# Optimization experiments

Measured on AMD Instinct MI355X. Metric: run time of the kernel, lower is better.

## Reference

```python
import jax, jax.numpy as jnp
import numpy as np

EPS = 1e-8
TOP_K = 3  # hardcoded in the original forward (torch.topk(sims, 3))


def setup_inputs() -> dict:
    key = jax.random.key(0)
    ks = jax.random.split(key, 6)
    n1, d1 = 4096, 1024
    n2, d2 = 4096, 4096
    V = jax.random.normal(ks[0], (n1, d1), dtype=jnp.float32)
    X = jax.random.normal(ks[1], (n2, d2), dtype=jnp.float32)
    # nn.Linear(visual_dim, text_dim): weight [d2, d1], bias [d2]
    Wv = jax.random.normal(ks[2], (d2, d1), dtype=jnp.float32) * (1.0 / np.sqrt(d1))
    bv = jax.random.normal(ks[3], (d2,), dtype=jnp.float32) * 0.01
    # nn.Linear(top_k, 1): weight [1, 3], bias [1]
    Wf = jax.random.normal(ks[4], (1, TOP_K), dtype=jnp.float32) * (1.0 / np.sqrt(TOP_K))
    bf = jax.random.normal(ks[5], (1,), dtype=jnp.float32) * 0.01
    return {"V": V, "X": X, "Wv": Wv, "bv": bv, "Wf": Wf, "bf": bf}


def reference(V, X, Wv, bv, Wf, bf):
    # project visual tokens into text space: [n1, d2]
    V_proj = V @ Wv.T + bv
    # cosine similarity: normalize queries (full-vector norm) and keys (row norm)
    Qn = X / (jnp.linalg.norm(X, axis=1, keepdims=True) + EPS)          # [n2, d2]
    Kn = V_proj / (jnp.linalg.norm(V_proj, axis=1, keepdims=True) + EPS)  # [n1, d2]
    sims = Qn @ Kn.T                                                     # [n2, n1]
    # per-text-token top-k visual tokens
    _, topk_idx = jax.lax.top_k(sims, TOP_K)                             # [n2, k]
    gathered = V_proj[topk_idx]                                          # [n2, k, d2]
    # fuse over k: Linear(k -> 1) applied along the top-k axis, squeeze -> [n2, d2]
    V_aligned = jnp.einsum('nkd,k->nd', gathered, Wf[0]) + bf[0]
    return jnp.concatenate([V_aligned, X], axis=0)                       # [2*n2, d2]
```

## Files before the change

kernel.cpp:

```cpp
#include <hip/hip_runtime.h>
#include <hip/hip_bf16.h>

constexpr int N1 = 4096;
constexpr int D1 = 1024;
constexpr int N2 = 4096;
constexpr int D2 = 4096;

#define FNEG  (-3.402823466e+38f)
#define IDX_INF 0x7FFFFFFF
#define NCHUNK 32
#define CPR (NCHUNK * 6)
#define FCAP 512
#define CERT_TH 1.5e-3f

using s16x8 = __attribute__((ext_vector_type(8))) short;
using f32x4 = __attribute__((ext_vector_type(4))) float;

static __device__ __forceinline__ unsigned short f2bf(float x) {
    unsigned int u = __float_as_uint(x);
    unsigned int r = (u + 0x7FFFu + ((u >> 16) & 1u)) >> 16;
    return (unsigned short)r;
}
static __device__ __forceinline__ float bf2f(unsigned short v) {
    return __uint_as_float((unsigned)v << 16);
}
static __device__ __forceinline__ void splitbf(float x, unsigned short& h,
                                               unsigned short& l) {
    unsigned short hh = f2bf(x);
    float r = x - __uint_as_float((unsigned)hh << 16);
    h = hh; l = f2bf(r);
}
static __device__ __forceinline__ int swz(int row, int g) {
    return row * 32 + ((g ^ (row & 3)) << 3);
}

static __device__ __forceinline__ void stageF32(const float* src, int ld,
    int rowbase, int k0, unsigned short* H, unsigned short* L, int tid)
{
    const int r = tid >> 1, half = tid & 1;
    const float* p = src + (size_t)(rowbase + r) * ld + k0 + half * 16;
#pragma unroll
    for (int gg = 0; gg < 2; ++gg) {
        const int g = half * 2 + gg;
        float4 v0 = *(const float4*)(p + gg * 8);
        float4 v1 = *(const float4*)(p + gg * 8 + 4);
        float xs[8] = {v0.x, v0.y, v0.z, v0.w, v1.x, v1.y, v1.z, v1.w};
        s16x8 hv, lv;
#pragma unroll
        for (int e = 0; e < 8; ++e) {
            unsigned short h, l; splitbf(xs[e], h, l);
            hv[e] = (short)h; lv[e] = (short)l;
        }
        const int a = swz(r, g);
        *(s16x8*)&H[a] = hv;
        *(s16x8*)&L[a] = lv;
    }
}

static __device__ __forceinline__ void gl_lds16(const void* g, void* l)
{
    __builtin_amdgcn_global_load_lds(
        (const __attribute__((address_space(1))) void*)g,
        (__attribute__((address_space(3))) void*)l, 16, 0, 0);
}

static __device__ __forceinline__ void stageSplitGL(const unsigned short* Hs,
    const unsigned short* Ls, int ld, int rowbase, int k0,
    unsigned short* H, unsigned short* L, int lane, int w)
{
#pragma unroll
    for (int t = 0; t < 2; ++t) {
        const int chunk = w * 128 + t * 64 + lane;
        const int row = chunk >> 2;
        const int gp  = chunk & 3;
        const int g   = gp ^ (row & 3);
        const unsigned short* sh =
            Hs + (size_t)(rowbase + row) * ld + k0 + g * 8;
        const unsigned short* sl =
            Ls + (size_t)(rowbase + row) * ld + k0 + g * 8;
        unsigned short* dh = H + (size_t)(w * 128 + t * 64) * 8;
        unsigned short* dl = L + (size_t)(w * 128 + t * 64) * 8;
        gl_lds16(sh, dh);
        gl_lds16(sl, dl);
    }
}

static __device__ __forceinline__ void stageWvTpre(const unsigned short* Wh,
    const unsigned short* Wl, int k0, int tn,
    unsigned short* H, unsigned short* L, int tid)
{
    const int kk = tid >> 3, cg = tid & 7;
    const int g = kk >> 3, idx = kk & 7;
    const unsigned short* ph = Wh + (size_t)(k0 + kk) * D1 + tn + cg * 16;
    const unsigned short* pl = Wl + (size_t)(k0 + kk) * D1 + tn + cg * 16;
#pragma unroll
    for (int q = 0; q < 4; ++q) {
        ushort4 vh = *(const ushort4*)(ph + q * 4);
        ushort4 vl = *(const ushort4*)(pl + q * 4);
        unsigned short hs[4] = {vh.x, vh.y, vh.z, vh.w};
        unsigned short ls[4] = {vl.x, vl.y, vl.z, vl.w};
#pragma unroll
        for (int e = 0; e < 4; ++e) {
            const int cc = cg * 16 + q * 4 + e;
            const int a = cc * 32 + ((g ^ (cc & 3)) << 3) + idx;
            H[a] = hs[e]; L[a] = ls[e];
        }
    }
}

static __device__ __forceinline__ s16x8 fragRead(const unsigned short* B,
                                                 int rowbase, int lane)
{
    const int row = rowbase + (lane & 15);
    const int g = lane >> 4;
    return *(const s16x8*)&B[row * 32 + ((g ^ (row & 3)) << 3)];
}

#define MFMA3(ACC, AH, AL, BH, BL)                                          \
    ACC = __builtin_amdgcn_mfma_f32_16x16x32_bf16(AH, BH, ACC, 0, 0, 0);    \
    ACC = __builtin_amdgcn_mfma_f32_16x16x32_bf16(AH, BL, ACC, 0, 0, 0);    \
    ACC = __builtin_amdgcn_mfma_f32_16x16x32_bf16(AL, BH, ACC, 0, 0, 0);

static __device__ __forceinline__ void top6f(float v, int i, float* vv, int* ii)
{
#pragma unroll
    for (int s = 0; s < 6; ++s) {
        if (v > vv[s]) {
#pragma unroll
            for (int t = 5; t > s; --t) { vv[t] = vv[t-1]; ii[t] = ii[t-1]; }
            vv[s] = v; ii[s] = i;
            break;
        }
    }
}

__global__ __launch_bounds__(256)
void kDetect(const float* c1, const float* c2, int* flags, int* flagCnt)
{
    __shared__ float red[256];
    float d = 0.f;
    for (int i = threadIdx.x; i < 4096; i += 256) {
        float a = c1[i], b = c2[i];
        d += a * a - b * b;
    }
    red[threadIdx.x] = d;
    __syncthreads();
    for (int st = 128; st > 0; st >>= 1) {
        if (threadIdx.x < st) red[threadIdx.x] += red[threadIdx.x + st];
        __syncthreads();
    }
    if (threadIdx.x == 0) {
        flags[0] = (red[0] < 0.f) ? 1 : 0;
        flagCnt[0] = 0;
    }
}

__global__ __launch_bounds__(256)
void kSplit(const float* src, unsigned short* h, unsigned short* l, int n4)
{
    int i = blockIdx.x * 256 + threadIdx.x;
    if (i >= n4) return;
    float4 v = *(const float4*)(src + (size_t)i * 4);
    float xs[4] = {v.x, v.y, v.z, v.w};
    ushort4 hv, lv;
    unsigned short hh, ll;
    splitbf(xs[0], hh, ll); hv.x = hh; lv.x = ll;
    splitbf(xs[1], hh, ll); hv.y = hh; lv.y = ll;
    splitbf(xs[2], hh, ll); hv.z = hh; lv.z = ll;
    splitbf(xs[3], hh, ll); hv.w = hh; lv.w = ll;
    *(ushort4*)(h + (size_t)i * 4) = hv;
    *(ushort4*)(l + (size_t)i * 4) = lv;
}

__global__ __launch_bounds__(256)
void kSvec(const float* X, const float* bv, float* sXF)
{
    __shared__ double red[256];
    const int row = blockIdx.x;
    double s = 0.0;
    for (int n = threadIdx.x; n < D2; n += 256)
        s += (double)X[(size_t)row * D2 + n] * (double)bv[n];
    red[threadIdx.x] = s;
    __syncthreads();
    for (int st = 128; st > 0; st >>= 1) {
        if (threadIdx.x < st) red[threadIdx.x] += red[threadIdx.x + st];
        __syncthreads();
    }
    if (threadIdx.x == 0) sXF[row] = (float)red[0];
}

__global__ __launch_bounds__(256)
void kNormMfma(const unsigned short* c1h, const unsigned short* c1l,
               const unsigned short* c2h, const unsigned short* c2l,
               const float* bv, const int* flags, float* partial,
               unsigned short* Vph)
{
    const unsigned short* Vh  = flags[0] ? c2h : c1h;
    const unsigned short* Vl  = flags[0] ? c2l : c1l;
    const unsigned short* Wvh = flags[0] ? c1h : c2h;
    const unsigned short* Wvl = flags[0] ? c1l : c2l;
    __shared__ unsigned short AH[4096], AL[4096], BH[4096], BL[4096];
    __shared__ float partH[128][2];
    const int tid = threadIdx.x;
    const int lane = tid & 63, w = tid >> 6;
    const int wr = w >> 1, wc = w & 1;
    const int tm = blockIdx.y * 128;
    const int tn = blockIdx.x * 128;

    f32x4 acc[4][4];
#pragma unroll
    for (int i = 0; i < 4; ++i)
#pragma unroll
        for (int j = 0; j < 4; ++j) acc[i][j] = (f32x4){0.f, 0.f, 0.f, 0.f};

    for (int k0 = 0; k0 < D1; k0 += 32) {
        stageSplitGL(Vh,  Vl,  D1, tm, k0, AH, AL, lane, w);
        stageSplitGL(Wvh, Wvl, D1, tn, k0, BH, BL, lane, w);
        __syncthreads();
        s16x8 ah[4], al[4], bh[4], bl[4];
#pragma unroll
        for (int f = 0; f < 4; ++f) {
            ah[f] = fragRead(AH, wr * 64 + f * 16, lane);
            al[f] = fragRead(AL, wr * 64 + f * 16, lane);
            bh[f] = fragRead(BH, wc * 64 + f * 16, lane);
            bl[f] = fragRead(BL, wc * 64 + f * 16, lane);
        }
#pragma unroll
        for (int fm = 0; fm < 4; ++fm)
#pragma unroll
            for (int fn = 0; fn < 4; ++fn) {
                MFMA3(acc[fm][fn], ah[fm], al[fm], bh[fn], bl[fn]);
            }
        __syncthreads();
    }

    float bvv[4];
#pragma unroll
    for (int fn = 0; fn < 4; ++fn)
        bvv[fn] = bv[tn + wc * 64 + fn * 16 + (lane & 15)];
#pragma unroll
    for (int fm = 0; fm < 4; ++fm)
#pragma unroll
        for (int r = 0; r < 4; ++r) {
            const int lrow = wr * 64 + fm * 16 + (lane >> 4) * 4 + r;
            float rs = 0.f;
#pragma unroll
            for (int fn = 0; fn < 4; ++fn) {
                float v = acc[fm][fn][r] + bvv[fn];
                Vph[(size_t)(tm + lrow) * D2 +
                    (tn + wc * 64 + fn * 16 + (lane & 15))] = f2bf(v);
                rs += v * v;
            }
            rs += __shfl_xor(rs, 1, 64);
            rs += __shfl_xor(rs, 2, 64);
            rs += __shfl_xor(rs, 4, 64);
            rs += __shfl_xor(rs, 8, 64);
            if ((lane & 15) == 0) partH[lrow][wc] = rs;
        }
    __syncthreads();
    if (tid < 128)
        partial[(size_t)(tm + tid) * 32 + blockIdx.x] =
            partH[tid][0] + partH[tid][1];
}

__global__ __launch_bounds__(256)
void kInv(const float* partial, float* invnF)
{
    int j = blockIdx.x * 256 + threadIdx.x;
    float s = 0.f;
    for (int cb = 0; cb < 32; ++cb) s += partial[(size_t)j * 32 + cb];
    invnF[j] = 1.f / (sqrtf(s) + 1e-8f);
}

__global__ __launch_bounds__(256)
void mfmaZ(const float* X,
           const unsigned short* c1h, const unsigned short* c1l,
           const unsigned short* c2h, const unsigned short* c2l,
           const int* flags, unsigned short* Zh, unsigned short* Zl)
{
    const unsigned short* Wvh = flags[0] ? c1h : c2h;
    const unsigned short* Wvl = flags[0] ? c1l : c2l;
    __shared__ unsigned short AH[4096], AL[4096], BH[4096], BL[4096];
    const int tid = threadIdx.x;
    const int lane = tid & 63, w = tid >> 6;
    const int wr = w >> 1, wc = w & 1;
    const int tm = blockIdx.y * 128;
    const int tn = blockIdx.x * 128;

    f32x4 acc[4][4];
#pragma unroll
    for (int i = 0; i < 4; ++i)
#pragma unroll
        for (int j = 0; j < 4; ++j) acc[i][j] = (f32x4){0.f, 0.f, 0.f, 0.f};

    for (int k0 = 0; k0 < D2; k0 += 32) {
        stageF32(X, D2, tm, k0, AH, AL, tid);
        stageWvTpre(Wvh, Wvl, k0, tn, BH, BL, tid);
        __syncthreads();
        s16x8 ah[4], al[4], bh[4], bl[4];
#pragma unroll
        for (int f = 0; f < 4; ++f) {
            ah[f] = fragRead(AH, wr * 64 + f * 16, lane);
            al[f] = fragRead(AL, wr * 64 + f * 16, lane);
            bh[f] = fragRead(BH, wc * 64 + f * 16, lane);
            bl[f] = fragRead(BL, wc * 64 + f * 16, lane);
        }
#pragma unroll
        for (int fm = 0; fm < 4; ++fm)
#pragma unroll
            for (int fn = 0; fn < 4; ++fn) {
                MFMA3(acc[fm][fn], ah[fm], al[fm], bh[fn], bl[fn]);
            }
        __syncthreads();
    }
#pragma unroll
    for (int fm = 0; fm < 4; ++fm)
#pragma unroll
        for (int fn = 0; fn < 4; ++fn)
#pragma unroll
            for (int r = 0; r < 4; ++r) {
                int row = tm + wr * 64 + fm * 16 + (lane >> 4) * 4 + r;
                int col = tn + wc * 64 + fn * 16 + (lane & 15);
                unsigned short h, l;
                splitbf(acc[fm][fn][r], h, l);
                size_t o = (size_t)row * D1 + col;
                Zh[o] = h; Zl[o] = l;
            }
}

__global__ __launch_bounds__(256)
void mfmaS(const unsigned short* Zh, const unsigned short* Zl,
           const unsigned short* c1h, const unsigned short* c1l,
           const unsigned short* c2h, const unsigned short* c2l,
           const float* invnF, const float* sXF, const int* flags,
           float* candV, int* candI)
{
    const unsigned short* Vh = flags[0] ? c2h : c1h;
    const unsigned short* Vl = flags[0] ? c2l : c1l;
    __shared__ __align__(16) char pool[41472];
    unsigned short* AH = (unsigned short*)pool;
    unsigned short* AL = (unsigned short*)(pool + 8192);
    unsigned short* BH = (unsigned short*)(pool + 16384);
    unsigned short* BL = (unsigned short*)(pool + 24576);
    float* Ct   = (float*)pool;
    float* pv   = (float*)(pool + 33792);
    int*   pi   = (int*)  (pool + 36864);
    float* invs = (float*)(pool + 39936);

    const int tid = threadIdx.x;
    const int lane = tid & 63, w = tid >> 6;
    const int wr = w >> 1, wc = w & 1;
    const int tm = blockIdx.y * 128;
    const int tn = blockIdx.x * 128;

    f32x4 acc[4][4];
#pragma unroll
    for (int i = 0; i < 4; ++i)
#pragma unroll
        for (int j = 0; j < 4; ++j) acc[i][j] = (f32x4){0.f, 0.f, 0.f, 0.f};

    for (int k0 = 0; k0 < D1; k0 += 32) {
        stageSplitGL(Zh, Zl, D1, tm, k0, AH, AL, lane, w);
        stageSplitGL(Vh, Vl, D1, tn, k0, BH, BL, lane, w);
        __syncthreads();
        s16x8 ah[4], al[4], bh[4], bl[4];
#pragma unroll
        for (int f = 0; f < 4; ++f) {
            ah[f] = fragRead(AH, wr * 64 + f * 16, lane);
            al[f] = fragRead(AL, wr * 64 + f * 16, lane);
            bh[f] = fragRead(BH, wc * 64 + f * 16, lane);
            bl[f] = fragRead(BL, wc * 64 + f * 16, lane);
        }
#pragma unroll
        for (int fm = 0; fm < 4; ++fm)
#pragma unroll
            for (int fn = 0; fn < 4; ++fn) {
                MFMA3(acc[fm][fn], ah[fm], al[fm], bh[fn], bl[fn]);
            }
        __syncthreads();
    }

    if (tid < 128) invs[tid] = invnF[tn + tid];
    for (int h = 0; h < 2; ++h) {
        __syncthreads();
        if (wr == h) {
#pragma unroll
            for (int fm = 0; fm < 4; ++fm)
#pragma unroll
                for (int fn = 0; fn < 4; ++fn)
#pragma unroll
                    for (int r = 0; r < 4; ++r) {
                        int lr = fm * 16 + (lane >> 4) * 4 + r;
                        int c  = wc * 64 + fn * 16 + (lane & 15);
                        Ct[lr * 132 + c] = acc[fm][fn][r];
                    }
        }
        __syncthreads();
        if (tid < 128) {
            int r = tid >> 1, seg = tid & 1;
            float sxf = sXF[tm + h * 64 + r];
            float vv[6]; int ii[6];
#pragma unroll
            for (int s = 0; s < 6; ++s) { vv[s] = FNEG; ii[s] = IDX_INF; }
            for (int cc = 0; cc < 64; ++cc) {
                int c = seg * 64 + cc;
                float v = (Ct[r * 132 + c] + sxf) * invs[c];
                top6f(v, tn + c, vv, ii);
            }
#pragma unroll
            for (int s = 0; s < 6; ++s) {
                pv[(r * 2 + seg) * 6 + s] = vv[s];
                pi[(r * 2 + seg) * 6 + s] = ii[s];
            }
        }
        __syncthreads();
        if (tid < 64) {
            float vv[6]; int ii[6];
#pragma unroll
            for (int s = 0; s < 6; ++s) { vv[s] = FNEG; ii[s] = IDX_INF; }
            for (int seg = 0; seg < 2; ++seg)
                for (int s = 0; s < 6; ++s)
                    top6f(pv[(tid * 2 + seg) * 6 + s],
                          pi[(tid * 2 + seg) * 6 + s], vv, ii);
            int row = tm + h * 64 + tid;
#pragma unroll
            for (int s = 0; s < 6; ++s) {
                candV[(size_t)row * CPR + blockIdx.x * 6 + s] = vv[s];
                candI[(size_t)row * CPR + blockIdx.x * 6 + s] = ii[s];
            }
        }
    }
}

__global__ __launch_bounds__(64)
void kMergeCert(const float* candV, const int* candI, int* tidx,
                int* flagCnt, int* flagRow, int* flagCand)
{
    if (threadIdx.x != 0) return;
    const int row = blockIdx.x;
    float vv[6]; int ii[6];
    for (int s = 0; s < 6; ++s) { vv[s] = FNEG; ii[s] = IDX_INF; }
    for (int c = 0; c < CPR; ++c)
        top6f(candV[(size_t)row * CPR + c], candI[(size_t)row * CPR + c],
              vv, ii);
    tidx[row * 3 + 0] = ii[0];
    tidx[row * 3 + 1] = ii[1];
    tidx[row * 3 + 2] = ii[2];
    bool cert = (vv[0] - vv[1] > CERT_TH) &&
                (vv[1] - vv[2] > CERT_TH) &&
                (vv[2] - vv[3] > CERT_TH);
    if (!cert) {
        int idx = atomicAdd(flagCnt, 1);
        if (idx < FCAP) {
            flagRow[idx] = row;
            for (int s = 0; s < 6; ++s) flagCand[idx * 6 + s] = ii[s];
        }
    }
}

__global__ __launch_bounds__(256)
void kExactPart(const int* flagCnt, const int* flagRow, const int* flagCand,
                const float* c1, const float* c2, const int* flags,
                const float* X, const float* bv, double* exPart)
{
    const int z = blockIdx.y;
    if (z >= flagCnt[0] || z >= FCAP) return;
    const float* V  = flags[0] ? c2 : c1;
    const float* Wv = flags[0] ? c1 : c2;
    const int row = flagRow[z];
    int js[6];
#pragma unroll
    for (int s = 0; s < 6; ++s) js[s] = flagCand[z * 6 + s];

    double dot[6] = {0,0,0,0,0,0}, nrm[6] = {0,0,0,0,0,0};
    const int nbase = blockIdx.x * 512;
#pragma unroll
    for (int t = 0; t < 2; ++t) {
        const int n = nbase + threadIdx.x * 2 + t;
        double v[6];
        const double bb = (double)bv[n];
#pragma unroll
        for (int s = 0; s < 6; ++s) v[s] = bb;
        const float* wrow = Wv + (size_t)n * D1;
        for (int k = 0; k < D1; ++k) {
            double wv = (double)wrow[k];
#pragma unroll
            for (int s = 0; s < 6; ++s)
                v[s] = fma((double)V[(size_t)js[s] * D1 + k], wv, v[s]);
        }
        const double xn = (double)X[(size_t)row * D2 + n];
#pragma unroll
        for (int s = 0; s < 6; ++s) {
            dot[s] = fma(xn, v[s], dot[s]);
            nrm[s] = fma(v[s], v[s], nrm[s]);
        }
    }
    __shared__ double red[256];
    for (int s = 0; s < 6; ++s) {
        red[threadIdx.x] = dot[s];
        __syncthreads();
        for (int st = 128; st > 0; st >>= 1) {
            if (threadIdx.x < st) red[threadIdx.x] += red[threadIdx.x + st];
            __syncthreads();
        }
        if (threadIdx.x == 0)
            exPart[(((size_t)z * 8 + blockIdx.x) * 6 + s) * 2 + 0] = red[0];
        __syncthreads();
        red[threadIdx.x] = nrm[s];
        __syncthreads();
        for (int st = 128; st > 0; st >>= 1) {
            if (threadIdx.x < st) red[threadIdx.x] += red[threadIdx.x + st];
            __syncthreads();
        }
        if (threadIdx.x == 0)
            exPart[(((size_t)z * 8 + blockIdx.x) * 6 + s) * 2 + 1] = red[0];
        __syncthreads();
    }
}

__global__ __launch_bounds__(64)
void kExactFinal(const int* flagCnt, const int* flagRow, const int* flagCand,
                 const double* exPart, int* tidx)
{
    const int z = blockIdx.x;
    if (z >= flagCnt[0] || z >= FCAP) return;
    if (threadIdx.x != 0) return;
    double sc[6]; int js[6];
    for (int s = 0; s < 6; ++s) {
        double dot = 0.0, nrm = 0.0;
        for (int c = 0; c < 8; ++c) {
            dot += exPart[(((size_t)z * 8 + c) * 6 + s) * 2 + 0];
            nrm += exPart[(((size_t)z * 8 + c) * 6 + s) * 2 + 1];
        }
        sc[s] = dot * (1.0 / (sqrt(nrm) + 1e-8));
        js[s] = flagCand[z * 6 + s];
    }
    int ord[6] = {0,1,2,3,4,5};
    for (int a = 0; a < 5; ++a)
        for (int b = a + 1; b < 6; ++b) {
            bool swp = (sc[ord[b]] > sc[ord[a]]) ||
                       (sc[ord[b]] == sc[ord[a]] && js[ord[b]] < js[ord[a]]);
            if (swp) { int t = ord[a]; ord[a] = ord[b]; ord[b] = t; }
        }
    const int row = flagRow[z];
    tidx[row * 3 + 0] = js[ord[0]];
    tidx[row * 3 + 1] = js[ord[1]];
    tidx[row * 3 + 2] = js[ord[2]];
}

__global__ __launch_bounds__(256)
void kGatherVa(const unsigned short* Vph, const int* tidx,
               const float* Wf, const float* bfp, float* outVa)
{
    const int row = blockIdx.x;
    const int i0 = tidx[row*3+0], i1 = tidx[row*3+1], i2 = tidx[row*3+2];
    const float w0 = Wf[0], w1 = Wf[1], w2 = Wf[2], b = bfp[0];
    const unsigned short* p0 = Vph + (size_t)i0 * D2;
    const unsigned short* p1 = Vph + (size_t)i1 * D2;
    const unsigned short* p2 = Vph + (size_t)i2 * D2;
    float* o = outVa + (size_t)row * D2;
    for (int c = threadIdx.x * 8; c < D2; c += 256 * 8) {
        s16x8 a = *(const s16x8*)(p0 + c);
        s16x8 d = *(const s16x8*)(p1 + c);
        s16x8 e = *(const s16x8*)(p2 + c);
        float out[8];
#pragma unroll
        for (int t = 0; t < 8; ++t)
            out[t] = w0 * bf2f((unsigned short)a[t]) +
                     w1 * bf2f((unsigned short)d[t]) +
                     w2 * bf2f((unsigned short)e[t]) + b;
        *(float4*)(o + c)     = *(float4*)&out[0];
        *(float4*)(o + c + 4) = *(float4*)&out[4];
    }
}

extern "C" void kernel_launch(void* const* d_in, const int* in_sizes, int n_in,
                              void* d_out, int out_size, void* d_ws, size_t ws_size,
                              hipStream_t stream)
{
    const float *c1 = nullptr, *c2 = nullptr, *X = nullptr;
    const float *bv = nullptr, *Wf = nullptr, *bfp = nullptr;
    for (int i = 0; i < n_in; ++i) {
        const float* p = (const float*)d_in[i];
        switch (in_sizes[i]) {
            case 16777216: X = p; break;
            case 4194304:  if (!c1) c1 = p; else c2 = p; break;
            case 4096:     bv = p; break;
            case 3:        Wf = p; break;
            case 1:        bfp = p; break;
            default: break;
        }
    }

    float* out_f = (float*)d_out;
    float* outVa = out_f;
    float* outX  = out_f + (size_t)N2 * D2;

    int* flags   = (int*)d_ws;
    int* flagCnt = (int*)((char*)d_ws + 128);
    char* C0 = (char*)d_ws + 1024;
    float* sXF     = (float*)(C0);
    float* invnF   = (float*)(C0 + 16384);
    int*   tidx    = (int*)  (C0 + 32768);
    float* aux2_unused = (float*)(C0 + 81920);
    float* partial = (float*)(C0 + 98304);
    float* candV   = (float*)(C0 + 622592);
    int*   candI   = (int*)  (C0 + 3768320);
    int*   flagRow = (int*)  (C0 + 6914048);
    int*   flagCand= (int*)  (C0 + 6916096);
    double* exPart = (double*)(C0 + 6928384);
    unsigned short* Zh = (unsigned short*)(C0 + 8388608);
    unsigned short* Zl = (unsigned short*)(C0 + 16777216);
    (void)aux2_unused;

    char* up = (char*)outX;
    unsigned short* c1h = (unsigned short*)(up);
    unsigned short* c1l = (unsigned short*)(up + 8388608);
    unsigned short* c2h = (unsigned short*)(up + 16777216);
    unsigned short* c2l = (unsigned short*)(up + 25165824);
    unsigned short* Vph = (unsigned short*)(up + 33554432);

    kDetect<<<1, 256, 0, stream>>>(c1, c2, flags, flagCnt);
    kSplit<<<4096, 256, 0, stream>>>(c1, c1h, c1l, N1 * D1 / 4);
    kSplit<<<4096, 256, 0, stream>>>(c2, c2h, c2l, N1 * D1 / 4);
    kSvec<<<N2, 256, 0, stream>>>(X, bv, sXF);

    dim3 gN(D2 / 128, N1 / 128);
    kNormMfma<<<gN, 256, 0, stream>>>(c1h, c1l, c2h, c2l, bv, flags,
                                      partial, Vph);
    kInv<<<16, 256, 0, stream>>>(partial, invnF);

    dim3 gZ(D1 / 128, N2 / 128);
    mfmaZ<<<gZ, 256, 0, stream>>>(X, c1h, c1l, c2h, c2l, flags, Zh, Zl);

    dim3 gS(N1 / 128, N2 / 128);
    mfmaS<<<gS, 256, 0, stream>>>(Zh, Zl, c1h, c1l, c2h, c2l,
                                  invnF, sXF, flags, candV, candI);

    kMergeCert<<<N2, 64, 0, stream>>>(candV, candI, tidx,
                                      flagCnt, flagRow, flagCand);
    dim3 gE(8, FCAP);
    kExactPart<<<gE, 256, 0, stream>>>(flagCnt, flagRow, flagCand,
                                       c1, c2, flags, X, bv, exPart);
    kExactFinal<<<FCAP, 64, 0, stream>>>(flagCnt, flagRow, flagCand,
                                         exPart, tidx);

    kGatherVa<<<N2, 256, 0, stream>>>(Vph, tidx, Wf, bfp, outVa);

    hipMemcpyAsync(outX, X, (size_t)N2 * D2 * sizeof(float),
                   hipMemcpyDeviceToDevice, stream);
}
```

Measured before the change: 1.577 ms.

## Double-buffer LDS tiles in split-bf16 MFMA GEMM kernels

Both split-precision GEMM kernels (the projection/norm kernel and the similarity kernel) now use two 32 KB LDS tile buffers in a 64 KB pool. The first K-slice is prefetched before the loop, and each iteration stages the next slice into the alternate buffer before running MFMAs on the current one. This drops the mid-iteration barrier and lets global loads overlap with matrix math. The cost is double the LDS per block, which may lower occupancy. The unused aux pointer is also removed.

New measurement: 1.542 ms. -2.2%, faster.

```diff
diff --git a/kernel.cpp b/kernel.cpp
--- a/kernel.cpp
+++ b/kernel.cpp
@@ -199,7 +199,7 @@
     const unsigned short* Vl  = flags[0] ? c2l : c1l;
     const unsigned short* Wvh = flags[0] ? c1h : c2h;
     const unsigned short* Wvl = flags[0] ? c1l : c2l;
-    __shared__ unsigned short AH[4096], AL[4096], BH[4096], BL[4096];
+    __shared__ __align__(16) char pool[65536];
     __shared__ float partH[128][2];
     const int tid = threadIdx.x;
     const int lane = tid & 63, w = tid >> 6;
@@ -213,17 +213,30 @@
 #pragma unroll
         for (int j = 0; j < 4; ++j) acc[i][j] = (f32x4){0.f, 0.f, 0.f, 0.f};
 
+    {
+        unsigned short* B0 = (unsigned short*)pool;
+        stageSplitGL(Vh,  Vl,  D1, tm, 0, B0,        B0 + 4096,  lane, w);
+        stageSplitGL(Wvh, Wvl, D1, tn, 0, B0 + 8192, B0 + 12288, lane, w);
+    }
+    __syncthreads();
+
     for (int k0 = 0; k0 < D1; k0 += 32) {
-        stageSplitGL(Vh,  Vl,  D1, tm, k0, AH, AL, lane, w);
-        stageSplitGL(Wvh, Wvl, D1, tn, k0, BH, BL, lane, w);
-        __syncthreads();
+        const int cur = (k0 >> 5) & 1;
+        unsigned short* CB = (unsigned short*)(pool + cur * 32768);
+        if (k0 + 32 < D1) {
+            unsigned short* NB = (unsigned short*)(pool + (cur ^ 1) * 32768);
+            stageSplitGL(Vh,  Vl,  D1, tm, k0 + 32, NB,        NB + 4096,
+                         lane, w);
+            stageSplitGL(Wvh, Wvl, D1, tn, k0 + 32, NB + 8192, NB + 12288,
+                         lane, w);
+        }
         s16x8 ah[4], al[4], bh[4], bl[4];
 #pragma unroll
         for (int f = 0; f < 4; ++f) {
-            ah[f] = fragRead(AH, wr * 64 + f * 16, lane);
-            al[f] = fragRead(AL, wr * 64 + f * 16, lane);
-            bh[f] = fragRead(BH, wc * 64 + f * 16, lane);
-            bl[f] = fragRead(BL, wc * 64 + f * 16, lane);
+            ah[f] = fragRead(CB,         wr * 64 + f * 16, lane);
+            al[f] = fragRead(CB + 4096,  wr * 64 + f * 16, lane);
+            bh[f] = fragRead(CB + 8192,  wc * 64 + f * 16, lane);
+            bl[f] = fragRead(CB + 12288, wc * 64 + f * 16, lane);
         }
 #pragma unroll
         for (int fm = 0; fm < 4; ++fm)
@@ -337,11 +350,7 @@
 {
     const unsigned short* Vh = flags[0] ? c2h : c1h;
     const unsigned short* Vl = flags[0] ? c2l : c1l;
-    __shared__ __align__(16) char pool[41472];
-    unsigned short* AH = (unsigned short*)pool;
-    unsigned short* AL = (unsigned short*)(pool + 8192);
-    unsigned short* BH = (unsigned short*)(pool + 16384);
-    unsigned short* BL = (unsigned short*)(pool + 24576);
+    __shared__ __align__(16) char pool[65536];
     float* Ct   = (float*)pool;
     float* pv   = (float*)(pool + 33792);
     int*   pi   = (int*)  (pool + 36864);
@@ -359,17 +368,30 @@
 #pragma unroll
         for (int j = 0; j < 4; ++j) acc[i][j] = (f32x4){0.f, 0.f, 0.f, 0.f};
 
+    {
+        unsigned short* B0 = (unsigned short*)pool;
+        stageSplitGL(Zh, Zl, D1, tm, 0, B0,        B0 + 4096,  lane, w);
+        stageSplitGL(Vh, Vl, D1, tn, 0, B0 + 8192, B0 + 12288, lane, w);
+    }
+    __syncthreads();
+
     for (int k0 = 0; k0 < D1; k0 += 32) {
-        stageSplitGL(Zh, Zl, D1, tm, k0, AH, AL, lane, w);
-        stageSplitGL(Vh, Vl, D1, tn, k0, BH, BL, lane, w);
-        __syncthreads();
+        const int cur = (k0 >> 5) & 1;
+        unsigned short* CB = (unsigned short*)(pool + cur * 32768);
+        if (k0 + 32 < D1) {
+            unsigned short* NB = (unsigned short*)(pool + (cur ^ 1) * 32768);
+            stageSplitGL(Zh, Zl, D1, tm, k0 + 32, NB,        NB + 4096,
+                         lane, w);
+            stageSplitGL(Vh, Vl, D1, tn, k0 + 32, NB + 8192, NB + 12288,
+                         lane, w);
+        }
         s16x8 ah[4], al[4], bh[4], bl[4];
 #pragma unroll
         for (int f = 0; f < 4; ++f) {
-            ah[f] = fragRead(AH, wr * 64 + f * 16, lane);
-            al[f] = fragRead(AL, wr * 64 + f * 16, lane);
-            bh[f] = fragRead(BH, wc * 64 + f * 16, lane);
-            bl[f] = fragRead(BL, wc * 64 + f * 16, lane);
+            ah[f] = fragRead(CB,         wr * 64 + f * 16, lane);
+            al[f] = fragRead(CB + 4096,  wr * 64 + f * 16, lane);
+            bh[f] = fragRead(CB + 8192,  wc * 64 + f * 16, lane);
+            bl[f] = fragRead(CB + 12288, wc * 64 + f * 16, lane);
         }
 #pragma unroll
         for (int fm = 0; fm < 4; ++fm)
@@ -602,7 +624,6 @@
     float* sXF     = (float*)(C0);
     float* invnF   = (float*)(C0 + 16384);
     int*   tidx    = (int*)  (C0 + 32768);
-    float* aux2_unused = (float*)(C0 + 81920);
     float* partial = (float*)(C0 + 98304);
     float* candV   = (float*)(C0 + 622592);
     int*   candI   = (int*)  (C0 + 3768320);
@@ -611,7 +632,6 @@
     double* exPart = (double*)(C0 + 6928384);
     unsigned short* Zh = (unsigned short*)(C0 + 8388608);
     unsigned short* Zl = (unsigned short*)(C0 + 16777216);
-    (void)aux2_unused;
 
     char* up = (char*)outX;
     unsigned short* c1h = (unsigned short*)(up);
```
